# Kernel optimization log

Hardware: AMD Instinct MI355X
Metric: run time of the kernel (lower is better)

The kernel has to match this reference:

```python
import jax, jax.numpy as jnp
import numpy as np

DT = 0.1
ROUTER_BLOCKS = 64
REPEAT = 64
IN_SIZE = 2048
HIDDEN = 4096
NNZ_W = int(IN_SIZE * HIDDEN * 0.01)   # 83886
NNZ_R = int(HIDDEN * HIDDEN * 0.01)    # 167772
BATCH = 512


def sparse_linear(x, rows, cols, vals, bias, out_features):
    """Edge-list sparse matmul: out[b, cols[e]] += x[b, rows[e]] * vals[e].
    Equivalent to torch.addmm(bias, x, W_csr) with W built from COO (coalesce
    sums duplicates; scatter-add does the same)."""
    contrib = x[:, rows] * vals  # [B, nnz]
    out = jnp.zeros((x.shape[0], out_features), x.dtype).at[:, cols].add(contrib)
    return out + bias


def setup_inputs() -> dict:
    key = jax.random.key(0)
    ks = jax.random.split(key, 20)
    inp = {}
    inp["x"] = jax.random.normal(ks[0], (BATCH, IN_SIZE), jnp.float32)
    inp["h_prev"] = jax.random.normal(ks[1], (BATCH, HIDDEN), jnp.float32)
    inp["gate"] = jax.random.uniform(ks[2], (BATCH, 1), jnp.float32)
    # SparseLinear params (init scale 1/sqrt(in_features), bias zeros)
    inp["W_vals"] = jax.random.normal(ks[3], (NNZ_W,), jnp.float32) / np.sqrt(IN_SIZE).astype(np.float32)
    inp["W_bias"] = jnp.zeros((HIDDEN,), jnp.float32)
    inp["R_vals"] = jax.random.normal(ks[4], (NNZ_R,), jnp.float32) / np.sqrt(HIDDEN).astype(np.float32)
    inp["R_bias"] = jnp.zeros((HIDDEN,), jnp.float32)
    inp["P_vals"] = jax.random.normal(ks[5], (NNZ_R,), jnp.float32) / np.sqrt(HIDDEN).astype(np.float32)
    inp["P_bias"] = jnp.zeros((HIDDEN,), jnp.float32)
    inp["router_w"] = jax.random.normal(ks[6], (ROUTER_BLOCKS, IN_SIZE), jnp.float32) / np.sqrt(IN_SIZE).astype(np.float32)
    inp["router_b"] = jnp.zeros((ROUTER_BLOCKS,), jnp.float32)
    # tau ~ U(0.1, 0.5) per TAU_CONCEPT_RANGE
    inp["tau"] = jax.random.uniform(ks[7], (HIDDEN,), jnp.float32) * 0.4 + 0.1
    # edge lists (int constants)
    inp["W_rows"] = jax.random.randint(ks[8], (NNZ_W,), 0, IN_SIZE, jnp.int32)
    inp["W_cols"] = jax.random.randint(ks[9], (NNZ_W,), 0, HIDDEN, jnp.int32)
    inp["R_rows"] = jax.random.randint(ks[10], (NNZ_R,), 0, HIDDEN, jnp.int32)
    inp["R_cols"] = jax.random.randint(ks[11], (NNZ_R,), 0, HIDDEN, jnp.int32)
    inp["P_rows"] = jax.random.randint(ks[12], (NNZ_R,), 0, HIDDEN, jnp.int32)
    inp["P_cols"] = jax.random.randint(ks[13], (NNZ_R,), 0, HIDDEN, jnp.int32)
    return inp


def reference(x, h_prev, gate, W_vals, W_bias, R_vals, R_bias, P_vals, P_bias,
              router_w, router_b, tau, W_rows, W_cols, R_rows, R_cols, P_rows, P_cols):
    r_gate = jax.nn.sigmoid(x @ router_w.T + router_b)            # [B, 64]
    mask = jnp.repeat(r_gate, REPEAT, axis=1)[:, :HIDDEN]          # [B, hidden]
    sensory = sparse_linear(x, W_rows, W_cols, W_vals, W_bias, HIDDEN) * mask
    rec = sparse_linear(h_prev, R_rows, R_cols, R_vals, R_bias, HIDDEN)
    target = jnp.tanh(sensory + rec)
    h_new = h_prev + gate * (target - h_prev) * (DT / tau)
    pred = sparse_linear(h_new, P_rows, P_cols, P_vals, P_bias, HIDDEN)
    return (h_new, pred)
```

## Files before the change

### kernel.cpp

```cpp
#include <hip/hip_runtime.h>
#include <math.h>

namespace {

constexpr int B     = 512;
constexpr int IN    = 2048;
constexpr int HID   = 4096;
constexpr int NNZ_W = 83886;
constexpr int NNZ_R = 167772;
constexpr int NTOT  = NNZ_W + 2 * NNZ_R;
constexpr int NCOLS = 3 * HID;
constexpr int SLOT  = 128;
constexpr float DT  = 0.1f;

typedef float f4 __attribute__((ext_vector_type(4)));
typedef float f2 __attribute__((ext_vector_type(2)));
typedef unsigned short us8 __attribute__((ext_vector_type(8)));

struct f8 { f4 lo, hi; };

__device__ __forceinline__ float bf2f(unsigned short u) {
  return __uint_as_float((unsigned int)u << 16);
}
__device__ __forceinline__ unsigned short f2bf(float f) {
  unsigned int u = __float_as_uint(f);
  u += 0x7FFFu + ((u >> 16) & 1u);
  return (unsigned short)(u >> 16);
}

__global__ void prep_k(const float* __restrict__ x, unsigned short* __restrict__ xTb,
                       const float* __restrict__ h, float* __restrict__ hT,
                       unsigned short* __restrict__ hTb,
                       const float* __restrict__ rw, const float* __restrict__ rb,
                       float* __restrict__ rgT, int* __restrict__ cnt) {
  __shared__ float sh[4 * IN];
  const int blk = blockIdx.x;
  const int tid = threadIdx.x;

  if (blk < 768) {
    const bool isX = blk < 256;
    const float* src; int C, tb;
    if (isX) { src = x; C = IN;  tb = blk; }
    else     { src = h; C = HID; tb = blk - 256; }
    const int tx_n = C / 64;
    const int bx = (tb % tx_n) * 64;
    const int by = (tb / tx_n) * 64;
    const int tx = tid & 63;
    const int ty = tid >> 6;
    for (int i = ty; i < 64; i += 8)
      sh[i * 65 + tx] = src[(size_t)(by + i) * C + bx + tx];
    __syncthreads();
    for (int i = ty; i < 64; i += 8) {
      const float v = sh[tx * 65 + i];
      const size_t di = (size_t)(bx + i) * B + by + tx;
      if (isX) xTb[di] = f2bf(v);
      else     { hT[di] = v; hTb[di] = f2bf(v); }
    }
  } else if (blk < 896) {
    const int b0 = (blk - 768) * 4;
    for (int k = tid; k < 4 * IN; k += 512) sh[k] = x[(size_t)b0 * IN + k];
    __syncthreads();
    const int wave = tid >> 6;
    const int lane = tid & 63;
#pragma unroll
    for (int j = 0; j < 8; ++j) {
      const int o = wave * 8 + j;
      const float* w = rw + (size_t)o * IN;
      float s0 = 0.f, s1 = 0.f, s2 = 0.f, s3 = 0.f;
      for (int i = 0; i < IN / 64; ++i) {
        const float wv = w[lane + 64 * i];
        s0 += sh[0 * IN + lane + 64 * i] * wv;
        s1 += sh[1 * IN + lane + 64 * i] * wv;
        s2 += sh[2 * IN + lane + 64 * i] * wv;
        s3 += sh[3 * IN + lane + 64 * i] * wv;
      }
#pragma unroll
      for (int d = 1; d < 64; d <<= 1) {
        s0 += __shfl_xor(s0, d);
        s1 += __shfl_xor(s1, d);
        s2 += __shfl_xor(s2, d);
        s3 += __shfl_xor(s3, d);
      }
      if (lane == 0) {
        const float bias = rb[o];
        rgT[o * B + b0 + 0] = 1.f / (1.f + expf(-(s0 + bias)));
        rgT[o * B + b0 + 1] = 1.f / (1.f + expf(-(s1 + bias)));
        rgT[o * B + b0 + 2] = 1.f / (1.f + expf(-(s2 + bias)));
        rgT[o * B + b0 + 3] = 1.f / (1.f + expf(-(s3 + bias)));
      }
    }
  } else {
    const int i = (blk - 896) * 512 + tid;
    if (i < NCOLS) cnt[i] = 0;
  }
}

__global__ void slotscat_k(const int* __restrict__ Wc, const int* __restrict__ Rc,
                           const int* __restrict__ Pc, const int* __restrict__ Wr,
                           const int* __restrict__ Rr, const int* __restrict__ Pr,
                           const float* __restrict__ Wv, const float* __restrict__ Rv,
                           const float* __restrict__ Pv, int* __restrict__ cnt,
                           float2* __restrict__ packed) {
  const int i = blockIdx.x * blockDim.x + threadIdx.x;
  if (i >= NTOT) return;
  int gc, r; float v;
  if (i < NNZ_W)              { gc = Wc[i];                 r = Wr[i]; v = Wv[i]; }
  else if (i < NNZ_W + NNZ_R) { int j = i - NNZ_W;          gc = HID + Rc[j];     r = Rr[j]; v = Rv[j]; }
  else                        { int j = i - NNZ_W - NNZ_R; gc = 2 * HID + Pc[j]; r = Pr[j]; v = Pv[j]; }
  const int p = atomicAdd(&cnt[gc], 1);
  packed[(size_t)gc * SLOT + p] = make_float2(v, __int_as_float(r));
}

__device__ __forceinline__ f8 gather_col_bf8(const unsigned short* __restrict__ srcb,
                                             const float2* __restrict__ packed,
                                             int gc, int n, int boff, float bias) {
  f4 a0; a0.x = bias; a0.y = bias; a0.z = bias; a0.w = bias;
  f4 a1 = a0;
  const f2* ep = (const f2*)(packed + (size_t)gc * SLOT);
  int i = 0;
  for (; i + 8 <= n; i += 8) {
    f2 e[8]; us8 s[8];
#pragma unroll
    for (int j = 0; j < 8; ++j) e[j] = ep[i + j];
#pragma unroll
    for (int j = 0; j < 8; ++j)
      s[j] = *(const us8*)(srcb + (size_t)__float_as_int(e[j].y) * B + boff);
#pragma unroll
    for (int j = 0; j < 8; ++j) {
      const float v = e[j].x;
      a0.x += v * bf2f(s[j][0]); a0.y += v * bf2f(s[j][1]);
      a0.z += v * bf2f(s[j][2]); a0.w += v * bf2f(s[j][3]);
      a1.x += v * bf2f(s[j][4]); a1.y += v * bf2f(s[j][5]);
      a1.z += v * bf2f(s[j][6]); a1.w += v * bf2f(s[j][7]);
    }
  }
  for (; i < n; ++i) {
    const f2 e = ep[i];
    const us8 s = *(const us8*)(srcb + (size_t)__float_as_int(e.y) * B + boff);
    const float v = e.x;
    a0.x += v * bf2f(s[0]); a0.y += v * bf2f(s[1]);
    a0.z += v * bf2f(s[2]); a0.w += v * bf2f(s[3]);
    a1.x += v * bf2f(s[4]); a1.y += v * bf2f(s[5]);
    a1.z += v * bf2f(s[6]); a1.w += v * bf2f(s[7]);
  }
  f8 r; r.lo = a0; r.hi = a1;
  return r;
}

__device__ __forceinline__ void store_tile_T(float* __restrict__ tile,
                                             const f8 v, int wave, int lane,
                                             int c0, float* __restrict__ out) {
  ((f4*)tile)[wave * 128 + lane * 2 + 0] = v.lo;
  ((f4*)tile)[wave * 128 + lane * 2 + 1] = v.hi;
  __syncthreads();
  const int t = threadIdx.x;
#pragma unroll
  for (int r = 0; r < 2; ++r) {
    const int b = r * 256 + t;
    f4 o;
    o.x = tile[0 * 512 + b];
    o.y = tile[1 * 512 + b];
    o.z = tile[2 * 512 + b];
    o.w = tile[3 * 512 + b];
    *(f4*)(out + (size_t)b * HID + c0) = o;
  }
}

__global__ void fused_gc_k(const unsigned short* __restrict__ xTb,
                           const unsigned short* __restrict__ hTb,
                           const float* __restrict__ hT,
                           const float2* __restrict__ packed, const int* __restrict__ cnt,
                           const float* __restrict__ rgT,
                           const float* __restrict__ gate, const float* __restrict__ tau,
                           const float* __restrict__ wb, const float* __restrict__ rb,
                           float* __restrict__ out_h, unsigned short* __restrict__ hnb) {
  __shared__ float tile[4 * 512];
  const int wave = threadIdx.x >> 6, lane = threadIdx.x & 63;
  const int c0 = blockIdx.x * 4;
  const int c = c0 + wave;
  const int boff = lane * 8;

  const f8 sens = gather_col_bf8(xTb, packed, c, cnt[c], boff, wb[c]);
  const f8 rec  = gather_col_bf8(hTb, packed, HID + c, cnt[HID + c], boff, rb[c]);

  const float* rg = rgT + (size_t)(c >> 6) * B + boff;
  const f4 m0 = *(const f4*)rg;
  const f4 m1 = *(const f4*)(rg + 4);
  const f4 g0 = *(const f4*)(gate + boff);
  const f4 g1 = *(const f4*)(gate + boff + 4);
  const float* hpp = hT + (size_t)c * B + boff;
  const f4 hp0 = *(const f4*)hpp;
  const f4 hp1 = *(const f4*)(hpp + 4);
  const float k = DT / tau[c];

  f8 hn;
  hn.lo.x = hp0.x + g0.x * (tanhf(sens.lo.x * m0.x + rec.lo.x) - hp0.x) * k;
  hn.lo.y = hp0.y + g0.y * (tanhf(sens.lo.y * m0.y + rec.lo.y) - hp0.y) * k;
  hn.lo.z = hp0.z + g0.z * (tanhf(sens.lo.z * m0.z + rec.lo.z) - hp0.z) * k;
  hn.lo.w = hp0.w + g0.w * (tanhf(sens.lo.w * m0.w + rec.lo.w) - hp0.w) * k;
  hn.hi.x = hp1.x + g1.x * (tanhf(sens.hi.x * m1.x + rec.hi.x) - hp1.x) * k;
  hn.hi.y = hp1.y + g1.y * (tanhf(sens.hi.y * m1.y + rec.hi.y) - hp1.y) * k;
  hn.hi.z = hp1.z + g1.z * (tanhf(sens.hi.z * m1.z + rec.hi.z) - hp1.z) * k;
  hn.hi.w = hp1.w + g1.w * (tanhf(sens.hi.w * m1.w + rec.hi.w) - hp1.w) * k;

  us8 hb;
  hb[0] = f2bf(hn.lo.x); hb[1] = f2bf(hn.lo.y); hb[2] = f2bf(hn.lo.z); hb[3] = f2bf(hn.lo.w);
  hb[4] = f2bf(hn.hi.x); hb[5] = f2bf(hn.hi.y); hb[6] = f2bf(hn.hi.z); hb[7] = f2bf(hn.hi.w);
  *(us8*)(hnb + (size_t)c * B + boff) = hb;

  store_tile_T(tile, hn, wave, lane, c0, out_h);
}

__global__ void pred_k(const unsigned short* __restrict__ hnb,
                       const float2* __restrict__ packed, const int* __restrict__ cnt,
                       const float* __restrict__ pb, float* __restrict__ out_p) {
  __shared__ float tile[4 * 512];
  const int wave = threadIdx.x >> 6, lane = threadIdx.x & 63;
  const int c0 = blockIdx.x * 4;
  const int c = c0 + wave;
  const int boff = lane * 8;
  const f8 p = gather_col_bf8(hnb, packed, 2 * HID + c, cnt[2 * HID + c], boff, pb[c]);
  store_tile_T(tile, p, wave, lane, c0, out_p);
}

}

extern "C" void kernel_launch(void* const* d_in, const int* in_sizes, int n_in,
                              void* d_out, int out_size, void* d_ws, size_t ws_size,
                              hipStream_t stream) {
  const float* x        = (const float*)d_in[0];
  const float* h_prev   = (const float*)d_in[1];
  const float* gate     = (const float*)d_in[2];
  const float* W_vals   = (const float*)d_in[3];
  const float* W_bias   = (const float*)d_in[4];
  const float* R_vals   = (const float*)d_in[5];
  const float* R_bias   = (const float*)d_in[6];
  const float* P_vals   = (const float*)d_in[7];
  const float* P_bias   = (const float*)d_in[8];
  const float* router_w = (const float*)d_in[9];
  const float* router_b = (const float*)d_in[10];
  const float* tau      = (const float*)d_in[11];
  const int* W_rows = (const int*)d_in[12];
  const int* W_cols = (const int*)d_in[13];
  const int* R_rows = (const int*)d_in[14];
  const int* R_cols = (const int*)d_in[15];
  const int* P_rows = (const int*)d_in[16];
  const int* P_cols = (const int*)d_in[17];

  float* ws = (float*)d_ws;
  unsigned short* xTb = (unsigned short*)ws;
  float*  hT     = ws + (size_t)IN * B / 2;
  unsigned short* hTb = (unsigned short*)(hT + (size_t)HID * B);
  float*  rgT    = (float*)(hTb + (size_t)HID * B);
  unsigned short* hnb = (unsigned short*)(rgT + 64 * B);
  float2* packed = (float2*)(hnb + (size_t)HID * B);
  int*    cnt    = (int*)(packed + (size_t)NCOLS * SLOT);

  float* out_h = (float*)d_out;
  float* out_p = out_h + (size_t)B * HID;

  prep_k<<<920, 512, 0, stream>>>(x, xTb, h_prev, hT, hTb,
                                  router_w, router_b, rgT, cnt);

  slotscat_k<<<(NTOT + 255) / 256, 256, 0, stream>>>(W_cols, R_cols, P_cols,
                                                     W_rows, R_rows, P_rows,
                                                     W_vals, R_vals, P_vals,
                                                     cnt, packed);

  fused_gc_k<<<HID / 4, 256, 0, stream>>>(xTb, hTb, hT, packed, cnt, rgT,
                                          gate, tau, W_bias, R_bias, out_h, hnb);

  pred_k<<<HID / 4, 256, 0, stream>>>(hnb, packed, cnt, P_bias, out_p);
}
```

Before: 98.89 us.

## Split each column's edge list across two waves and reduce partial sums in LDS

Both gather kernels now use 512-thread blocks in which two waves share each output column, each walking half of that column's edge list and storing partial sums to shared memory. After a barrier, each thread handles one batch row, adds the two halves plus the bias, and applies the epilogue (tanh update, bf16 write, output store). The aim is to double the waves available to hide gather latency and shorten each wave's serial loop. In exchange it uses more LDS, a block-wide barrier and a reduction step, and launch_bounds(512,1) may limit occupancy.

```diff
diff --git a/kernel.cpp b/kernel.cpp
--- a/kernel.cpp
+++ b/kernel.cpp
@@ -111,14 +111,14 @@
   packed[(size_t)gc * SLOT + p] = make_float2(v, __int_as_float(r));
 }
 
-__device__ __forceinline__ f8 gather_col_bf8(const unsigned short* __restrict__ srcb,
-                                             const float2* __restrict__ packed,
-                                             int gc, int n, int boff, float bias) {
-  f4 a0; a0.x = bias; a0.y = bias; a0.z = bias; a0.w = bias;
+__device__ __forceinline__ f8 gather_part(const unsigned short* __restrict__ srcb,
+                                          const float2* __restrict__ packed,
+                                          int gc, int beg, int end, int boff) {
+  f4 a0; a0.x = 0.f; a0.y = 0.f; a0.z = 0.f; a0.w = 0.f;
   f4 a1 = a0;
   const f2* ep = (const f2*)(packed + (size_t)gc * SLOT);
-  int i = 0;
-  for (; i + 8 <= n; i += 8) {
+  int i = beg;
+  for (; i + 8 <= end; i += 8) {
     f2 e[8]; us8 s[8];
 #pragma unroll
     for (int j = 0; j < 8; ++j) e[j] = ep[i + j];
@@ -134,7 +134,7 @@
       a1.z += v * bf2f(s[j][6]); a1.w += v * bf2f(s[j][7]);
     }
   }
-  for (; i < n; ++i) {
+  for (; i < end; ++i) {
     const f2 e = ep[i];
     const us8 s = *(const us8*)(srcb + (size_t)__float_as_int(e.y) * B + boff);
     const float v = e.x;
@@ -147,80 +147,88 @@
   return r;
 }
 
-__device__ __forceinline__ void store_tile_T(float* __restrict__ tile,
-                                             const f8 v, int wave, int lane,
-                                             int c0, float* __restrict__ out) {
-  ((f4*)tile)[wave * 128 + lane * 2 + 0] = v.lo;
-  ((f4*)tile)[wave * 128 + lane * 2 + 1] = v.hi;
+__device__ __forceinline__ void put_part(float* __restrict__ tile,
+                                         int w, int lane, const f8 v) {
+  *(f4*)(tile + w * 512 + lane * 8)     = v.lo;
+  *(f4*)(tile + w * 512 + lane * 8 + 4) = v.hi;
+}
+
+__global__ void __launch_bounds__(512, 1)
+fused_gc_k(const unsigned short* __restrict__ xTb,
+           const unsigned short* __restrict__ hTb,
+           const float* __restrict__ hT,
+           const float2* __restrict__ packed, const int* __restrict__ cnt,
+           const float* __restrict__ rgT,
+           const float* __restrict__ gate, const float* __restrict__ tau,
+           const float* __restrict__ wb, const float* __restrict__ rb,
+           float* __restrict__ out_h, unsigned short* __restrict__ hnb) {
+  __shared__ float sT[8 * 512];
+  __shared__ float rT[8 * 512];
+  const int tid  = threadIdx.x;
+  const int w    = tid >> 6;
+  const int lane = tid & 63;
+  const int half = w & 1;
+  const int c0   = blockIdx.x * 4;
+  const int c    = c0 + (w >> 1);
+  const int boff = lane * 8;
+
+  const int nW = cnt[c];
+  const int bW = half ? nW / 2 : 0;
+  const int eW = half ? nW : nW / 2;
+  put_part(sT, w, lane, gather_part(xTb, packed, c, bW, eW, boff));
+
+  const int nR = cnt[HID + c];
+  const int bR = half ? nR / 2 : 0;
+  const int eR = half ? nR : nR / 2;
+  put_part(rT, w, lane, gather_part(hTb, packed, HID + c, bR, eR, boff));
+
   __syncthreads();
-  const int t = threadIdx.x;
-#pragma unroll
-  for (int r = 0; r < 2; ++r) {
-    const int b = r * 256 + t;
-    f4 o;
-    o.x = tile[0 * 512 + b];
-    o.y = tile[1 * 512 + b];
-    o.z = tile[2 * 512 + b];
-    o.w = tile[3 * 512 + b];
-    *(f4*)(out + (size_t)b * HID + c0) = o;
-  }
-}
-
-__global__ void fused_gc_k(const unsigned short* __restrict__ xTb,
-                           const unsigned short* __restrict__ hTb,
-                           const float* __restrict__ hT,
-                           const float2* __restrict__ packed, const int* __restrict__ cnt,
-                           const float* __restrict__ rgT,
-                           const float* __restrict__ gate, const float* __restrict__ tau,
-                           const float* __restrict__ wb, const float* __restrict__ rb,
-                           float* __restrict__ out_h, unsigned short* __restrict__ hnb) {
-  __shared__ float tile[4 * 512];
-  const int wave = threadIdx.x >> 6, lane = threadIdx.x & 63;
-  const int c0 = blockIdx.x * 4;
-  const int c = c0 + wave;
+
+  const int b = tid;
+  const float m = rgT[(size_t)(c0 >> 6) * B + b];
+  const float g = gate[b];
+  f4 o;
+#pragma unroll
+  for (int cc = 0; cc < 4; ++cc) {
+    const int c2 = c0 + cc;
+    const float sens = sT[(2 * cc) * 512 + b] + sT[(2 * cc + 1) * 512 + b] + wb[c2];
+    const float rec  = rT[(2 * cc) * 512 + b] + rT[(2 * cc + 1) * 512 + b] + rb[c2];
+    const float hp   = hT[(size_t)c2 * B + b];
+    const float hn   = hp + g * (tanhf(sens * m + rec) - hp) * (DT / tau[c2]);
+    hnb[(size_t)c2 * B + b] = f2bf(hn);
+    ((float*)&o)[cc] = hn;
+  }
+  *(f4*)(out_h + (size_t)b * HID + c0) = o;
+}
+
+__global__ void __launch_bounds__(512, 1)
+pred_k(const unsigned short* __restrict__ hnb,
+       const float2* __restrict__ packed, const int* __restrict__ cnt,
+       const float* __restrict__ pb, float* __restrict__ out_p) {
+  __shared__ float pT[8 * 512];
+  const int tid  = threadIdx.x;
+  const int w    = tid >> 6;
+  const int lane = tid & 63;
+  const int half = w & 1;
+  const int c0   = blockIdx.x * 4;
+  const int c    = c0 + (w >> 1);
   const int boff = lane * 8;
 
-  const f8 sens = gather_col_bf8(xTb, packed, c, cnt[c], boff, wb[c]);
-  const f8 rec  = gather_col_bf8(hTb, packed, HID + c, cnt[HID + c], boff, rb[c]);
-
-  const float* rg = rgT + (size_t)(c >> 6) * B + boff;
-  const f4 m0 = *(const f4*)rg;
-  const f4 m1 = *(const f4*)(rg + 4);
-  const f4 g0 = *(const f4*)(gate + boff);
-  const f4 g1 = *(const f4*)(gate + boff + 4);
-  const float* hpp = hT + (size_t)c * B + boff;
-  const f4 hp0 = *(const f4*)hpp;
-  const f4 hp1 = *(const f4*)(hpp + 4);
-  const float k = DT / tau[c];
-
-  f8 hn;
-  hn.lo.x = hp0.x + g0.x * (tanhf(sens.lo.x * m0.x + rec.lo.x) - hp0.x) * k;
-  hn.lo.y = hp0.y + g0.y * (tanhf(sens.lo.y * m0.y + rec.lo.y) - hp0.y) * k;
-  hn.lo.z = hp0.z + g0.z * (tanhf(sens.lo.z * m0.z + rec.lo.z) - hp0.z) * k;
-  hn.lo.w = hp0.w + g0.w * (tanhf(sens.lo.w * m0.w + rec.lo.w) - hp0.w) * k;
-  hn.hi.x = hp1.x + g1.x * (tanhf(sens.hi.x * m1.x + rec.hi.x) - hp1.x) * k;
-  hn.hi.y = hp1.y + g1.y * (tanhf(sens.hi.y * m1.y + rec.hi.y) - hp1.y) * k;
-  hn.hi.z = hp1.z + g1.z * (tanhf(sens.hi.z * m1.z + rec.hi.z) - hp1.z) * k;
-  hn.hi.w = hp1.w + g1.w * (tanhf(sens.hi.w * m1.w + rec.hi.w) - hp1.w) * k;
-
-  us8 hb;
-  hb[0] = f2bf(hn.lo.x); hb[1] = f2bf(hn.lo.y); hb[2] = f2bf(hn.lo.z); hb[3] = f2bf(hn.lo.w);
-  hb[4] = f2bf(hn.hi.x); hb[5] = f2bf(hn.hi.y); hb[6] = f2bf(hn.hi.z); hb[7] = f2bf(hn.hi.w);
-  *(us8*)(hnb + (size_t)c * B + boff) = hb;
-
-  store_tile_T(tile, hn, wave, lane, c0, out_h);
-}
-
-__global__ void pred_k(const unsigned short* __restrict__ hnb,
-                       const float2* __restrict__ packed, const int* __restrict__ cnt,
-                       const float* __restrict__ pb, float* __restrict__ out_p) {
-  __shared__ float tile[4 * 512];
-  const int wave = threadIdx.x >> 6, lane = threadIdx.x & 63;
-  const int c0 = blockIdx.x * 4;
-  const int c = c0 + wave;
-  const int boff = lane * 8;
-  const f8 p = gather_col_bf8(hnb, packed, 2 * HID + c, cnt[2 * HID + c], boff, pb[c]);
-  store_tile_T(tile, p, wave, lane, c0, out_p);
+  const int nP = cnt[2 * HID + c];
+  const int bP = half ? nP / 2 : 0;
+  const int eP = half ? nP : nP / 2;
+  put_part(pT, w, lane, gather_part(hnb, packed, 2 * HID + c, bP, eP, boff));
+
+  __syncthreads();
+
+  const int b = tid;
+  f4 o;
+#pragma unroll
+  for (int cc = 0; cc < 4; ++cc) {
+    const int c2 = c0 + cc;
+    ((float*)&o)[cc] = pT[(2 * cc) * 512 + b] + pT[(2 * cc + 1) * 512 + b] + pb[c2];
+  }
+  *(f4*)(out_p + (size_t)b * HID + c0) = o;
 }
 
 }
@@ -267,8 +275,8 @@
                                                      W_vals, R_vals, P_vals,
                                                      cnt, packed);
 
-  fused_gc_k<<<HID / 4, 256, 0, stream>>>(xTb, hTb, hT, packed, cnt, rgT,
+  fused_gc_k<<<HID / 4, 512, 0, stream>>>(xTb, hTb, hT, packed, cnt, rgT,
                                           gate, tau, W_bias, R_bias, out_h, hnb);
 
-  pred_k<<<HID / 4, 256, 0, stream>>>(hnb, packed, cnt, P_bias, out_p);
-}
+  pred_k<<<HID / 4, 512, 0, stream>>>(hnb, packed, cnt, P_bias, out_p);
+}
```

Measured after the change: 117.5 us. +18.8%, slower.
